# Performance work log

Hardware: AMD Instinct MI355X
Metric: run time of the kernel (lower is better)

## Reference

```python
import jax, jax.numpy as jnp
import numpy as np

N_NODES = 100000
N_EDGES = 640000
LATDIM = 128
GNN_LAYER = 3
LN_EPS = 1e-5


def setup_inputs() -> dict:
    key = jax.random.key(0)
    k1, k2, k3, k4 = jax.random.split(key, 4)
    embeds = jax.random.normal(k1, (N_NODES, LATDIM), dtype=jnp.float32)
    adj_row = jax.random.randint(k2, (N_EDGES,), 0, N_NODES, dtype=jnp.int32)
    adj_col = jax.random.randint(k3, (N_EDGES,), 0, N_NODES, dtype=jnp.int32)
    adj_val = jax.random.uniform(k4, (N_EDGES,), dtype=jnp.float32)
    return {"embeds": embeds, "adj_row": adj_row, "adj_col": adj_col, "adj_val": adj_val}


def _layer_norm(x):
    # nn.LayerNorm(latdim, elementwise_affine=False)
    mu = jnp.mean(x, axis=-1, keepdims=True)
    var = jnp.mean(jnp.square(x - mu), axis=-1, keepdims=True)
    return (x - mu) / jnp.sqrt(var + LN_EPS)


def _spmm(adj_row, adj_col, adj_val, x):
    # out[r] += val * x[c] for each edge (r, c, val)  -- sparse [N,N] @ [N,d]
    msgs = adj_val[:, None] * x[adj_col]  # [E, d]
    return jax.ops.segment_sum(msgs, adj_row, num_segments=N_NODES)


def reference(embeds, adj_row, adj_col, adj_val):
    x = _layer_norm(embeds)
    acc = jnp.zeros_like(x)  # gnn_layer > 0, so hop-0 embeds are NOT included
    for _ in range(GNN_LAYER):
        x = _spmm(adj_row, adj_col, adj_val, x)
        acc = acc + x
    return acc
```

## Files before the change

kernel.cpp:

```cpp
#include <hip/hip_runtime.h>

#define N_NODES 100000
#define N_EDGES 640000
#define LATDIM  128
#define LN_EPS  1e-5f

typedef unsigned int u32;

#define SCAN_NB   98
#define N_PAD     (SCAN_NB * 1024)

__device__ __forceinline__ float bflo(u32 u) { return __uint_as_float(u << 16); }
__device__ __forceinline__ float bfhi(u32 u) { return __uint_as_float(u & 0xffff0000u); }
__device__ __forceinline__ u32 pack_bf2(float a, float b) {
    u32 ua = __float_as_uint(a), ub = __float_as_uint(b);
    ua = (ua + 0x7fffu + ((ua >> 16) & 1u)) >> 16;
    ub = (ub + 0x7fffu + ((ub >> 16) & 1u)) >> 16;
    return ua | (ub << 16);
}

__global__ __launch_bounds__(256) void ln_bf16_kernel(const float* __restrict__ in,
                                                      u32* __restrict__ out) {
    int tid  = threadIdx.x;
    int wave = tid >> 6;
    int lane = tid & 63;
    int half = lane >> 5;
    int sub  = lane & 31;
    int row  = blockIdx.x * 8 + wave * 2 + half;
    float4 v = ((const float4*)in)[(size_t)row * 32 + sub];
    float s  = v.x + v.y + v.z + v.w;
    float ss = v.x * v.x + v.y * v.y + v.z * v.z + v.w * v.w;
    #pragma unroll
    for (int o = 16; o > 0; o >>= 1) {
        s  += __shfl_xor(s,  o, 64);
        ss += __shfl_xor(ss, o, 64);
    }
    float mu   = s * (1.0f / LATDIM);
    float var  = ss * (1.0f / LATDIM) - mu * mu;
    float rstd = rsqrtf(var + LN_EPS);
    uint2 w;
    w.x = pack_bf2((v.x - mu) * rstd, (v.y - mu) * rstd);
    w.y = pack_bf2((v.z - mu) * rstd, (v.w - mu) * rstd);
    ((uint2*)out)[(size_t)row * 32 + sub] = w;
}

__global__ __launch_bounds__(256) void hist_kernel(const int* __restrict__ rowi,
                                                   int* __restrict__ cnt) {
    int e = blockIdx.x * 256 + threadIdx.x;
    if (e < N_EDGES) atomicAdd(&cnt[rowi[e]], 1);
}

__global__ __launch_bounds__(256) void scan_a_kernel(int* __restrict__ cnt,
                                                     int* __restrict__ bsums) {
    __shared__ int ts[256];
    int t = threadIdx.x;
    int base = blockIdx.x * 1024 + t * 4;
    int4 v = *(const int4*)(cnt + base);
    int s = v.x + v.y + v.z + v.w;
    ts[t] = s;
    __syncthreads();
    #pragma unroll
    for (int o = 1; o < 256; o <<= 1) {
        int u = 0;
        if (t >= o) u = ts[t - o];
        __syncthreads();
        if (t >= o) ts[t] += u;
        __syncthreads();
    }
    int excl = ts[t] - s;
    int4 w;
    w.x = excl;
    w.y = excl + v.x;
    w.z = excl + v.x + v.y;
    w.w = excl + v.x + v.y + v.z;
    *(int4*)(cnt + base) = w;
    if (t == 255) bsums[blockIdx.x] = ts[255];
}

__global__ __launch_bounds__(128) void scan_b_kernel(int* __restrict__ bsums) {
    __shared__ int ss[128];
    int t = threadIdx.x;
    int own = (t < SCAN_NB) ? bsums[t] : 0;
    ss[t] = own;
    __syncthreads();
    #pragma unroll
    for (int o = 1; o < 128; o <<= 1) {
        int u = 0;
        if (t >= o) u = ss[t - o];
        __syncthreads();
        if (t >= o) ss[t] += u;
        __syncthreads();
    }
    if (t < SCAN_NB) bsums[t] = ss[t] - own;
}

__global__ __launch_bounds__(256) void scan_c_kernel(int* __restrict__ cnt,
                                                     const int* __restrict__ bsums) {
    int off = bsums[blockIdx.x];
    int base = blockIdx.x * 1024 + threadIdx.x * 4;
    int4 v = *(const int4*)(cnt + base);
    v.x += off; v.y += off; v.z += off; v.w += off;
    *(int4*)(cnt + base) = v;
}

__global__ __launch_bounds__(256) void scatter_kernel(const int* __restrict__ rowi,
                                                      const int* __restrict__ coli,
                                                      const float* __restrict__ vali,
                                                      int* __restrict__ cursor,
                                                      int2* __restrict__ pairs) {
    int e = blockIdx.x * 256 + threadIdx.x;
    if (e >= N_EDGES) return;
    int r = rowi[e];
    int pos = atomicAdd(&cursor[r], 1);
    pairs[pos] = make_int2(coli[e], __float_as_int(vali[e]));
}

__global__ __launch_bounds__(256) void spmm_csr_kernel(const int* __restrict__ row_end,
                                                       const int2* __restrict__ pairs,
                                                       const u32* __restrict__ x,
                                                       u32* __restrict__ y,
                                                       const u32* __restrict__ add0,
                                                       const u32* __restrict__ add1,
                                                       float* __restrict__ out,
                                                       int mode) {
    int tid  = threadIdx.x;
    int wave = tid >> 6;
    int lane = tid & 63;
    int row  = blockIdx.x * 16 + wave * 4 + (lane >> 4);
    int sub  = lane & 15;
    int end   = row_end[row];
    int e     = row ? row_end[row - 1] : 0;
    const uint4* x4 = (const uint4*)x;
    float a0=0,a1=0,a2=0,a3=0,a4=0,a5=0,a6=0,a7=0;
    for (; e < end; ++e) {
        int2 p = pairs[e];
        uint4 g = x4[(size_t)p.x * 16 + sub];
        float v = __int_as_float(p.y);
        a0 += v * bflo(g.x); a1 += v * bfhi(g.x);
        a2 += v * bflo(g.y); a3 += v * bfhi(g.y);
        a4 += v * bflo(g.z); a5 += v * bfhi(g.z);
        a6 += v * bflo(g.w); a7 += v * bfhi(g.w);
    }
    size_t oi = (size_t)row * 16 + sub;
    if (mode == 2) {
        uint4 b0 = ((const uint4*)add0)[oi];
        uint4 b1 = ((const uint4*)add1)[oi];
        a0 += bflo(b0.x) + bflo(b1.x); a1 += bfhi(b0.x) + bfhi(b1.x);
        a2 += bflo(b0.y) + bflo(b1.y); a3 += bfhi(b0.y) + bfhi(b1.y);
        a4 += bflo(b0.z) + bflo(b1.z); a5 += bfhi(b0.z) + bfhi(b1.z);
        a6 += bflo(b0.w) + bflo(b1.w); a7 += bfhi(b0.w) + bfhi(b1.w);
        float4* o4 = (float4*)(out + (size_t)row * LATDIM + sub * 8);
        o4[0] = make_float4(a0, a1, a2, a3);
        o4[1] = make_float4(a4, a5, a6, a7);
    } else {
        uint4 w;
        w.x = pack_bf2(a0, a1);
        w.y = pack_bf2(a2, a3);
        w.z = pack_bf2(a4, a5);
        w.w = pack_bf2(a6, a7);
        ((uint4*)y)[oi] = w;
    }
}

__global__ __launch_bounds__(256) void ln_f32_kernel(const float* __restrict__ in,
                                                     float* __restrict__ out) {
    int tid  = threadIdx.x;
    int wave = tid >> 6;
    int lane = tid & 63;
    int half = lane >> 5;
    int sub  = lane & 31;
    int row  = blockIdx.x * 8 + wave * 2 + half;
    if (row >= N_NODES) return;
    float4 v = ((const float4*)in)[(size_t)row * 32 + sub];
    float s  = v.x + v.y + v.z + v.w;
    float ss = v.x * v.x + v.y * v.y + v.z * v.z + v.w * v.w;
    #pragma unroll
    for (int o = 16; o > 0; o >>= 1) {
        s  += __shfl_xor(s,  o, 64);
        ss += __shfl_xor(ss, o, 64);
    }
    float mu   = s * (1.0f / LATDIM);
    float var  = ss * (1.0f / LATDIM) - mu * mu;
    float rstd = rsqrtf(var + LN_EPS);
    float4 o4;
    o4.x = (v.x - mu) * rstd; o4.y = (v.y - mu) * rstd;
    o4.z = (v.z - mu) * rstd; o4.w = (v.w - mu) * rstd;
    ((float4*)out)[(size_t)row * 32 + sub] = o4;
}

__global__ __launch_bounds__(256) void spmm_atomic_kernel(const int* __restrict__ rowi,
                                                          const int* __restrict__ coli,
                                                          const float* __restrict__ vali,
                                                          const float* __restrict__ x,
                                                          float* __restrict__ y) {
    int t = blockIdx.x * 256 + threadIdx.x;
    int e = t >> 5;
    if (e >= N_EDGES) return;
    int k = t & 31;
    int r = rowi[e];
    int c = coli[e];
    float v = vali[e];
    float4 xv = ((const float4*)(x + (size_t)c * LATDIM))[k];
    float* yp = y + (size_t)r * LATDIM + k * 4;
    atomicAdd(yp + 0, v * xv.x);
    atomicAdd(yp + 1, v * xv.y);
    atomicAdd(yp + 2, v * xv.z);
    atomicAdd(yp + 3, v * xv.w);
}

__global__ __launch_bounds__(256) void addz_kernel(float* __restrict__ acc,
                                                   const float* __restrict__ x,
                                                   float* __restrict__ z,
                                                   int first) {
    size_t i = (size_t)blockIdx.x * 256 + threadIdx.x;
    float4 xv = ((const float4*)x)[i];
    float4* ap = ((float4*)acc) + i;
    if (first) {
        *ap = xv;
    } else {
        float4 a = *ap;
        a.x += xv.x; a.y += xv.y; a.z += xv.z; a.w += xv.w;
        *ap = a;
    }
    if (z) ((float4*)z)[i] = make_float4(0.f, 0.f, 0.f, 0.f);
}

extern "C" void kernel_launch(void* const* d_in, const int* in_sizes, int n_in,
                              void* d_out, int out_size, void* d_ws, size_t ws_size,
                              hipStream_t stream) {
    const float* embeds  = (const float*)d_in[0];
    const int*   adj_row = (const int*)d_in[1];
    const int*   adj_col = (const int*)d_in[2];
    const float* adj_val = (const float*)d_in[3];
    float* out = (float*)d_out;

    u32*  A16  = (u32*)d_ws;
    u32*  B16  = A16 + (size_t)N_NODES * (LATDIM / 2);
    int*  cnt   = (int*)(B16 + (size_t)N_NODES * (LATDIM / 2));
    int*  bsums = cnt + N_PAD;
    int2* pairs = (int2*)(bsums + 128);
    size_t need = (size_t)((char*)(pairs + N_EDGES) - (char*)d_ws);

    const int lnGrid   = N_NODES / 8;
    const int edgeGrid = (N_EDGES + 255) / 256;
    const int rowGrid  = N_NODES / 16;

    if (ws_size >= need) {
        ln_bf16_kernel<<<lnGrid, 256, 0, stream>>>(embeds, A16);
        hipMemsetAsync(cnt, 0, (size_t)N_PAD * sizeof(int), stream);
        hist_kernel<<<edgeGrid, 256, 0, stream>>>(adj_row, cnt);
        scan_a_kernel<<<SCAN_NB, 256, 0, stream>>>(cnt, bsums);
        scan_b_kernel<<<1, 128, 0, stream>>>(bsums);
        scan_c_kernel<<<SCAN_NB, 256, 0, stream>>>(cnt, bsums);
        scatter_kernel<<<edgeGrid, 256, 0, stream>>>(adj_row, adj_col, adj_val,
                                                     cnt, pairs);
        spmm_csr_kernel<<<rowGrid, 256, 0, stream>>>(cnt, pairs, A16, B16,
                                                     nullptr, nullptr, nullptr, 0);
        spmm_csr_kernel<<<rowGrid, 256, 0, stream>>>(cnt, pairs, B16, A16,
                                                     nullptr, nullptr, nullptr, 0);
        spmm_csr_kernel<<<rowGrid, 256, 0, stream>>>(cnt, pairs, A16, nullptr,
                                                     B16, A16, out, 2);
    } else {
        float* A = (float*)d_ws;
        float* B = A + (size_t)N_NODES * LATDIM;
        const size_t rowBytes = (size_t)N_NODES * LATDIM * sizeof(float);
        const int spmmGrid = (N_EDGES * 32 + 255) / 256;
        const int addGrid  = (N_NODES * LATDIM / 4 + 255) / 256;
        ln_f32_kernel<<<lnGrid, 256, 0, stream>>>(embeds, A);
        hipMemsetAsync(B, 0, rowBytes, stream);
        spmm_atomic_kernel<<<spmmGrid, 256, 0, stream>>>(adj_row, adj_col, adj_val, A, B);
        addz_kernel<<<addGrid, 256, 0, stream>>>(out, B, A, 1);
        spmm_atomic_kernel<<<spmmGrid, 256, 0, stream>>>(adj_row, adj_col, adj_val, B, A);
        addz_kernel<<<addGrid, 256, 0, stream>>>(out, A, B, 0);
        spmm_atomic_kernel<<<spmmGrid, 256, 0, stream>>>(adj_row, adj_col, adj_val, A, B);
        addz_kernel<<<addGrid, 256, 0, stream>>>(out, B, nullptr, 0);
    }
}
```

Before: 282.2 us.

## Fuse LN with histogram, merge scan stages, unroll SpMM gather loop

```diff
diff --git a/kernel.cpp b/kernel.cpp
--- a/kernel.cpp
+++ b/kernel.cpp
@@ -6,9 +6,13 @@
 #define LN_EPS  1e-5f
 
 typedef unsigned int u32;
+typedef float f32x4 __attribute__((ext_vector_type(4)));
 
 #define SCAN_NB   98
 #define N_PAD     (SCAN_NB * 1024)
+
+#define LN_BLOCKS   (N_NODES / 8)
+#define HIST_BLOCKS ((N_EDGES + 255) / 256)
 
 __device__ __forceinline__ float bflo(u32 u) { return __uint_as_float(u << 16); }
 __device__ __forceinline__ float bfhi(u32 u) { return __uint_as_float(u & 0xffff0000u); }
@@ -19,40 +23,44 @@
     return ua | (ub << 16);
 }
 
-__global__ __launch_bounds__(256) void ln_bf16_kernel(const float* __restrict__ in,
-                                                      u32* __restrict__ out) {
-    int tid  = threadIdx.x;
-    int wave = tid >> 6;
-    int lane = tid & 63;
-    int half = lane >> 5;
-    int sub  = lane & 31;
-    int row  = blockIdx.x * 8 + wave * 2 + half;
-    float4 v = ((const float4*)in)[(size_t)row * 32 + sub];
-    float s  = v.x + v.y + v.z + v.w;
-    float ss = v.x * v.x + v.y * v.y + v.z * v.z + v.w * v.w;
-    #pragma unroll
-    for (int o = 16; o > 0; o >>= 1) {
-        s  += __shfl_xor(s,  o, 64);
-        ss += __shfl_xor(ss, o, 64);
-    }
-    float mu   = s * (1.0f / LATDIM);
-    float var  = ss * (1.0f / LATDIM) - mu * mu;
-    float rstd = rsqrtf(var + LN_EPS);
-    uint2 w;
-    w.x = pack_bf2((v.x - mu) * rstd, (v.y - mu) * rstd);
-    w.y = pack_bf2((v.z - mu) * rstd, (v.w - mu) * rstd);
-    ((uint2*)out)[(size_t)row * 32 + sub] = w;
-}
-
-__global__ __launch_bounds__(256) void hist_kernel(const int* __restrict__ rowi,
-                                                   int* __restrict__ cnt) {
-    int e = blockIdx.x * 256 + threadIdx.x;
-    if (e < N_EDGES) atomicAdd(&cnt[rowi[e]], 1);
-}
-
-__global__ __launch_bounds__(256) void scan_a_kernel(int* __restrict__ cnt,
-                                                     int* __restrict__ bsums) {
+__global__ __launch_bounds__(256) void ln_hist_kernel(const float* __restrict__ in,
+                                                      u32* __restrict__ out,
+                                                      const int* __restrict__ rowi,
+                                                      int* __restrict__ cnt) {
+    int b = blockIdx.x;
+    if (b < LN_BLOCKS) {
+        int tid  = threadIdx.x;
+        int wave = tid >> 6;
+        int lane = tid & 63;
+        int half = lane >> 5;
+        int sub  = lane & 31;
+        int row  = b * 8 + wave * 2 + half;
+        f32x4 v = __builtin_nontemporal_load(((const f32x4*)in) + (size_t)row * 32 + sub);
+        float s  = v.x + v.y + v.z + v.w;
+        float ss = v.x * v.x + v.y * v.y + v.z * v.z + v.w * v.w;
+        #pragma unroll
+        for (int o = 16; o > 0; o >>= 1) {
+            s  += __shfl_xor(s,  o, 64);
+            ss += __shfl_xor(ss, o, 64);
+        }
+        float mu   = s * (1.0f / LATDIM);
+        float var  = ss * (1.0f / LATDIM) - mu * mu;
+        float rstd = rsqrtf(var + LN_EPS);
+        uint2 w;
+        w.x = pack_bf2((v.x - mu) * rstd, (v.y - mu) * rstd);
+        w.y = pack_bf2((v.z - mu) * rstd, (v.w - mu) * rstd);
+        ((uint2*)out)[(size_t)row * 32 + sub] = w;
+    } else {
+        int e = (b - LN_BLOCKS) * 256 + threadIdx.x;
+        if (e < N_EDGES) atomicAdd(&cnt[rowi[e]], 1);
+    }
+}
+
+__global__ __launch_bounds__(256) void scan_ab_kernel(int* __restrict__ cnt,
+                                                      int* __restrict__ bsums,
+                                                      int* __restrict__ done) {
     __shared__ int ts[256];
+    __shared__ int amLast;
     int t = threadIdx.x;
     int base = blockIdx.x * 1024 + t * 4;
     int4 v = *(const int4*)(cnt + base);
@@ -74,48 +82,51 @@
     w.z = excl + v.x + v.y;
     w.w = excl + v.x + v.y + v.z;
     *(int4*)(cnt + base) = w;
-    if (t == 255) bsums[blockIdx.x] = ts[255];
-}
-
-__global__ __launch_bounds__(128) void scan_b_kernel(int* __restrict__ bsums) {
-    __shared__ int ss[128];
-    int t = threadIdx.x;
-    int own = (t < SCAN_NB) ? bsums[t] : 0;
-    ss[t] = own;
+    if (t == 255) {
+        __hip_atomic_store(&bsums[blockIdx.x], ts[255],
+                           __ATOMIC_RELEASE, __HIP_MEMORY_SCOPE_AGENT);
+        int prev = __hip_atomic_fetch_add(done, 1,
+                                          __ATOMIC_ACQ_REL, __HIP_MEMORY_SCOPE_AGENT);
+        amLast = (prev == SCAN_NB - 1);
+    }
     __syncthreads();
-    #pragma unroll
-    for (int o = 1; o < 128; o <<= 1) {
-        int u = 0;
-        if (t >= o) u = ss[t - o];
+    if (amLast) {
+        __shared__ int ss[128];
+        int own = 0;
+        if (t < 128) {
+            own = (t < SCAN_NB)
+                ? __hip_atomic_load(&bsums[t], __ATOMIC_ACQUIRE, __HIP_MEMORY_SCOPE_AGENT)
+                : 0;
+            ss[t] = own;
+        }
         __syncthreads();
-        if (t >= o) ss[t] += u;
-        __syncthreads();
-    }
-    if (t < SCAN_NB) bsums[t] = ss[t] - own;
-}
-
-__global__ __launch_bounds__(256) void scan_c_kernel(int* __restrict__ cnt,
-                                                     const int* __restrict__ bsums) {
-    int off = bsums[blockIdx.x];
-    int base = blockIdx.x * 1024 + threadIdx.x * 4;
-    int4 v = *(const int4*)(cnt + base);
-    v.x += off; v.y += off; v.z += off; v.w += off;
-    *(int4*)(cnt + base) = v;
+        #pragma unroll
+        for (int o = 1; o < 128; o <<= 1) {
+            int u = 0;
+            if (t >= o && t < 128) u = ss[t - o];
+            __syncthreads();
+            if (t >= o && t < 128) ss[t] += u;
+            __syncthreads();
+        }
+        if (t < SCAN_NB) bsums[t] = ss[t] - own;
+    }
 }
 
 __global__ __launch_bounds__(256) void scatter_kernel(const int* __restrict__ rowi,
                                                       const int* __restrict__ coli,
                                                       const float* __restrict__ vali,
                                                       int* __restrict__ cursor,
+                                                      const int* __restrict__ bsums,
                                                       int2* __restrict__ pairs) {
     int e = blockIdx.x * 256 + threadIdx.x;
     if (e >= N_EDGES) return;
     int r = rowi[e];
-    int pos = atomicAdd(&cursor[r], 1);
+    int pos = atomicAdd(&cursor[r], 1) + bsums[r >> 10];
     pairs[pos] = make_int2(coli[e], __float_as_int(vali[e]));
 }
 
 __global__ __launch_bounds__(256) void spmm_csr_kernel(const int* __restrict__ row_end,
+                                                       const int* __restrict__ bsums,
                                                        const int2* __restrict__ pairs,
                                                        const u32* __restrict__ x,
                                                        u32* __restrict__ y,
@@ -128,11 +139,27 @@
     int lane = tid & 63;
     int row  = blockIdx.x * 16 + wave * 4 + (lane >> 4);
     int sub  = lane & 15;
-    int end   = row_end[row];
-    int e     = row ? row_end[row - 1] : 0;
+    int end = row_end[row] + bsums[row >> 10];
+    int e   = row ? row_end[row - 1] + bsums[(row - 1) >> 10] : 0;
     const uint4* x4 = (const uint4*)x;
     float a0=0,a1=0,a2=0,a3=0,a4=0,a5=0,a6=0,a7=0;
-    for (; e < end; ++e) {
+    for (; e + 2 <= end; e += 2) {
+        int2 p0 = pairs[e];
+        int2 p1 = pairs[e + 1];
+        uint4 g0 = x4[(size_t)p0.x * 16 + sub];
+        uint4 g1 = x4[(size_t)p1.x * 16 + sub];
+        float v0 = __int_as_float(p0.y);
+        float v1 = __int_as_float(p1.y);
+        a0 += v0 * bflo(g0.x); a1 += v0 * bfhi(g0.x);
+        a2 += v0 * bflo(g0.y); a3 += v0 * bfhi(g0.y);
+        a4 += v0 * bflo(g0.z); a5 += v0 * bfhi(g0.z);
+        a6 += v0 * bflo(g0.w); a7 += v0 * bfhi(g0.w);
+        a0 += v1 * bflo(g1.x); a1 += v1 * bfhi(g1.x);
+        a2 += v1 * bflo(g1.y); a3 += v1 * bfhi(g1.y);
+        a4 += v1 * bflo(g1.z); a5 += v1 * bfhi(g1.z);
+        a6 += v1 * bflo(g1.w); a7 += v1 * bfhi(g1.w);
+    }
+    if (e < end) {
         int2 p = pairs[e];
         uint4 g = x4[(size_t)p.x * 16 + sub];
         float v = __int_as_float(p.y);
@@ -149,9 +176,11 @@
         a2 += bflo(b0.y) + bflo(b1.y); a3 += bfhi(b0.y) + bfhi(b1.y);
         a4 += bflo(b0.z) + bflo(b1.z); a5 += bfhi(b0.z) + bfhi(b1.z);
         a6 += bflo(b0.w) + bflo(b1.w); a7 += bfhi(b0.w) + bfhi(b1.w);
-        float4* o4 = (float4*)(out + (size_t)row * LATDIM + sub * 8);
-        o4[0] = make_float4(a0, a1, a2, a3);
-        o4[1] = make_float4(a4, a5, a6, a7);
+        f32x4* o4 = (f32x4*)(out + (size_t)row * LATDIM + sub * 8);
+        f32x4 r0 = {a0, a1, a2, a3};
+        f32x4 r1 = {a4, a5, a6, a7};
+        __builtin_nontemporal_store(r0, o4 + 0);
+        __builtin_nontemporal_store(r1, o4 + 1);
     } else {
         uint4 w;
         w.x = pack_bf2(a0, a1);
@@ -238,27 +267,25 @@
     u32*  B16  = A16 + (size_t)N_NODES * (LATDIM / 2);
     int*  cnt   = (int*)(B16 + (size_t)N_NODES * (LATDIM / 2));
     int*  bsums = cnt + N_PAD;
-    int2* pairs = (int2*)(bsums + 128);
+    int*  done  = bsums + 128;
+    int2* pairs = (int2*)(done + 32);
     size_t need = (size_t)((char*)(pairs + N_EDGES) - (char*)d_ws);
 
-    const int lnGrid   = N_NODES / 8;
     const int edgeGrid = (N_EDGES + 255) / 256;
     const int rowGrid  = N_NODES / 16;
 
     if (ws_size >= need) {
-        ln_bf16_kernel<<<lnGrid, 256, 0, stream>>>(embeds, A16);
-        hipMemsetAsync(cnt, 0, (size_t)N_PAD * sizeof(int), stream);
-        hist_kernel<<<edgeGrid, 256, 0, stream>>>(adj_row, cnt);
-        scan_a_kernel<<<SCAN_NB, 256, 0, stream>>>(cnt, bsums);
-        scan_b_kernel<<<1, 128, 0, stream>>>(bsums);
-        scan_c_kernel<<<SCAN_NB, 256, 0, stream>>>(cnt, bsums);
+        hipMemsetAsync(cnt, 0, (size_t)(N_PAD + 128 + 32) * sizeof(int), stream);
+        ln_hist_kernel<<<LN_BLOCKS + HIST_BLOCKS, 256, 0, stream>>>(embeds, A16,
+                                                                    adj_row, cnt);
+        scan_ab_kernel<<<SCAN_NB, 256, 0, stream>>>(cnt, bsums, done);
         scatter_kernel<<<edgeGrid, 256, 0, stream>>>(adj_row, adj_col, adj_val,
-                                                     cnt, pairs);
-        spmm_csr_kernel<<<rowGrid, 256, 0, stream>>>(cnt, pairs, A16, B16,
+                                                     cnt, bsums, pairs);
+        spmm_csr_kernel<<<rowGrid, 256, 0, stream>>>(cnt, bsums, pairs, A16, B16,
                                                      nullptr, nullptr, nullptr, 0);
-        spmm_csr_kernel<<<rowGrid, 256, 0, stream>>>(cnt, pairs, B16, A16,
+        spmm_csr_kernel<<<rowGrid, 256, 0, stream>>>(cnt, bsums, pairs, B16, A16,
                                                      nullptr, nullptr, nullptr, 0);
-        spmm_csr_kernel<<<rowGrid, 256, 0, stream>>>(cnt, pairs, A16, nullptr,
+        spmm_csr_kernel<<<rowGrid, 256, 0, stream>>>(cnt, bsums, pairs, A16, nullptr,
                                                      B16, A16, out, 2);
     } else {
         float* A = (float*)d_ws;
@@ -266,7 +293,7 @@
         const size_t rowBytes = (size_t)N_NODES * LATDIM * sizeof(float);
         const int spmmGrid = (N_EDGES * 32 + 255) / 256;
         const int addGrid  = (N_NODES * LATDIM / 4 + 255) / 256;
-        ln_f32_kernel<<<lnGrid, 256, 0, stream>>>(embeds, A);
+        ln_f32_kernel<<<LN_BLOCKS, 256, 0, stream>>>(embeds, A);
         hipMemsetAsync(B, 0, rowBytes, stream);
         spmm_atomic_kernel<<<spmmGrid, 256, 0, stream>>>(adj_row, adj_col, adj_val, A, B);
         addz_kernel<<<addGrid, 256, 0, stream>>>(out, B, A, 1);
```

Result: no change. 279.2 us (-1.1%).
